# Optimization experiments

Hardware: AMD Instinct MI355X
Metric: run time of the kernel (lower is better)

## Reference

```python
import jax, jax.numpy as jnp
import numpy as np

NEG_INF = -9e15
NEG_SLOPE = 0.2

def setup_inputs() -> dict:
    key = jax.random.key(0)
    k1, k2, k3, k4 = jax.random.split(key, 4)
    N, d_in, d_out = 8192, 256, 256
    x = jax.random.normal(k1, (N, d_in), dtype=jnp.float32)
    adj = jax.random.randint(k2, (N, N), 0, 2).astype(jnp.float32)
    W = jax.random.normal(k3, (d_in, d_out), dtype=jnp.float32) * (1.0 / np.sqrt(d_in))
    a = jax.random.normal(k4, (2 * d_out,), dtype=jnp.float32) * (1.0 / np.sqrt(2 * d_out))
    return {"x": x, "adj": adj, "W": W, "a": a}

def reference(x, adj, W, a):
    d_out = W.shape[1]
    Wh = x @ W                                   # [N, d_out]
    # a([Wh_i || Wh_j]) decomposed: e_ij = <a_src, Wh_i> + <a_dst, Wh_j>
    e_src = Wh @ a[:d_out]                       # [N]
    e_dst = Wh @ a[d_out:]                       # [N]
    e = jax.nn.leaky_relu(e_src[:, None] + e_dst[None, :], NEG_SLOPE)  # [N, N]
    N = Wh.shape[0]
    mask = (adj > 0) | jnp.eye(N, dtype=bool)
    e = jnp.where(mask, e, NEG_INF)
    alpha = jax.nn.softmax(e, axis=1)            # [N, N]
    h = alpha @ Wh                               # [N, d_out]
    return h
```

## Files before the change

kernel.cpp:

```cpp
#include <hip/hip_runtime.h>
#include <stdint.h>

#define N 8192
#define D 256

typedef __attribute__((ext_vector_type(4))) float f32x4;
typedef __attribute__((ext_vector_type(8))) short bf16x8;

__device__ __forceinline__ unsigned short f2bf(float f) {
    unsigned u = __float_as_uint(f);
    u += 0x7fff + ((u >> 16) & 1);
    return (unsigned short)(u >> 16);
}
__device__ __forceinline__ float bf2f(unsigned short h) {
    unsigned u = ((unsigned)h) << 16;
    return __uint_as_float(u);
}
__device__ __forceinline__ float leaky(float x) {
    return fmaxf(x, 0.f) + 0.2f * fminf(x, 0.f);
}
__device__ __forceinline__ void sync_lds() {
    asm volatile("s_waitcnt lgkmcnt(0)\n\ts_barrier" ::: "memory");
}

__global__ __launch_bounds__(256) void k0_compress(const float* __restrict__ adj,
                                                   unsigned int* __restrict__ mask) {
    const size_t fbase = ((size_t)blockIdx.x * 256 + threadIdx.x) * 4;
    float4 v = *(const float4*)(adj + fbase);
    const int lane = threadIdx.x & 63;
    unsigned nib = (v.x > 0.f ? 1u : 0u) | (v.y > 0.f ? 2u : 0u) |
                   (v.z > 0.f ? 4u : 0u) | (v.w > 0.f ? 8u : 0u);
    unsigned word = nib << ((lane & 7) * 4);
    word |= __shfl_xor(word, 1);
    word |= __shfl_xor(word, 2);
    word |= __shfl_xor(word, 4);
    if ((lane & 7) == 0) {
        size_t widx = fbase >> 5;
        int r = (int)(widx >> 8);
        int ww = (int)(widx & 255);
        if ((r >> 5) == ww) word |= 1u << (r & 31);
        mask[widx] = word;
    }
}

__global__ __launch_bounds__(256) void k1c_x(const float* __restrict__ x,
                                             unsigned short* __restrict__ xhi,
                                             unsigned short* __restrict__ xlo) {
    const size_t idx = ((size_t)blockIdx.x * 256 + threadIdx.x) * 4;
    float4 v = *(const float4*)(x + idx);
    unsigned short h[4], l[4];
    float vv[4] = {v.x, v.y, v.z, v.w};
#pragma unroll
    for (int j = 0; j < 4; ++j) {
        h[j] = f2bf(vv[j]);
        l[j] = f2bf(vv[j] - bf2f(h[j]));
    }
    *(ushort4*)(xhi + idx) = *(ushort4*)h;
    *(ushort4*)(xlo + idx) = *(ushort4*)l;
}

__global__ __launch_bounds__(256) void k1w(const float* __restrict__ W,
                                           unsigned short* __restrict__ wthi,
                                           unsigned short* __restrict__ wtlo) {
    const int n = blockIdx.x;
    const int k = threadIdx.x;
    float w = W[(size_t)k * D + n];
    unsigned short h = f2bf(w);
    unsigned short l = f2bf(w - bf2f(h));
    wthi[(size_t)n * D + k] = h;
    wtlo[(size_t)n * D + k] = l;
}

__global__ __launch_bounds__(256) void k1m(const unsigned short* __restrict__ xhi,
                                           const unsigned short* __restrict__ xlo,
                                           const unsigned short* __restrict__ wthi,
                                           const unsigned short* __restrict__ wtlo,
                                           const float* __restrict__ a,
                                           unsigned short* __restrict__ WhT,
                                           float* __restrict__ e_src,
                                           float* __restrict__ e_dst) {
    __shared__ float obuf[16 * 256];

    const int t = threadIdx.x;
    const int r0 = blockIdx.x * 16;
    const int w = t >> 6;
    const int lane = t & 63;
    const int quad = lane >> 4, lo = lane & 15;

    const unsigned short* xh_row = xhi + (size_t)(r0 + lo) * D;
    const unsigned short* xl_row = xlo + (size_t)(r0 + lo) * D;

    f32x4 acc[4];
#pragma unroll
    for (int nt = 0; nt < 4; ++nt) acc[nt] = (f32x4){0.f, 0.f, 0.f, 0.f};

#pragma unroll
    for (int ks = 0; ks < 8; ++ks) {
        const int kofs = ks * 32 + quad * 8;
        bf16x8 ah = *(const bf16x8*)(xh_row + kofs);
        bf16x8 al = *(const bf16x8*)(xl_row + kofs);
#pragma unroll
        for (int nt = 0; nt < 4; ++nt) {
            const int n = w * 64 + nt * 16 + lo;
            bf16x8 bh = *(const bf16x8*)(wthi + (size_t)n * D + kofs);
            bf16x8 bl = *(const bf16x8*)(wtlo + (size_t)n * D + kofs);
            acc[nt] = __builtin_amdgcn_mfma_f32_16x16x32_bf16(ah, bh, acc[nt], 0, 0, 0);
            acc[nt] = __builtin_amdgcn_mfma_f32_16x16x32_bf16(ah, bl, acc[nt], 0, 0, 0);
            acc[nt] = __builtin_amdgcn_mfma_f32_16x16x32_bf16(al, bh, acc[nt], 0, 0, 0);
        }
    }

#pragma unroll
    for (int nt = 0; nt < 4; ++nt) {
        const int n = w * 64 + nt * 16 + lo;
        unsigned short pk[4];
#pragma unroll
        for (int reg = 0; reg < 4; ++reg) pk[reg] = f2bf(acc[nt][reg]);
        *(ushort2*)(WhT + (size_t)n * N + r0 + quad * 4) = *(ushort2*)&pk[0];
        *(ushort2*)(WhT + (size_t)n * N + r0 + quad * 4 + 2) = *(ushort2*)&pk[2];
    }

#pragma unroll
    for (int nt = 0; nt < 4; ++nt) {
        const int col = w * 64 + nt * 16 + lo;
#pragma unroll
        for (int reg = 0; reg < 4; ++reg)
            obuf[(quad * 4 + reg) * 256 + col] = acc[nt][reg];
    }
    __syncthreads();

    const int row = t >> 4;
    const int c0 = (t & 15) * 16;
    float ps = 0.f, pd = 0.f;
#pragma unroll
    for (int j = 0; j < 4; ++j) {
        float4 wv = *(const float4*)&obuf[row * 256 + c0 + j * 4];
        float4 as = *(const float4*)(a + c0 + j * 4);
        float4 ad = *(const float4*)(a + D + c0 + j * 4);
        ps += wv.x * as.x + wv.y * as.y + wv.z * as.z + wv.w * as.w;
        pd += wv.x * ad.x + wv.y * ad.y + wv.z * ad.z + wv.w * ad.w;
    }
#pragma unroll
    for (int msk = 1; msk < 16; msk <<= 1) {
        ps += __shfl_xor(ps, msk);
        pd += __shfl_xor(pd, msk);
    }
    if ((t & 15) == 0) {
        e_src[r0 + row] = ps;
        e_dst[r0 + row] = pd;
    }
}

__global__ __launch_bounds__(256) void k3_max(const float* __restrict__ e_dst,
                                              float* __restrict__ maxdst) {
    __shared__ float red[4];
    const int t = threadIdx.x;
    float m = -3.4e38f;
    for (int i = t; i < N; i += 256) m = fmaxf(m, e_dst[i]);
#pragma unroll
    for (int msk = 1; msk < 64; msk <<= 1) m = fmaxf(m, __shfl_xor(m, msk));
    if ((t & 63) == 0) red[t >> 6] = m;
    __syncthreads();
    if (t == 0) *maxdst = fmaxf(fmaxf(red[0], red[1]), fmaxf(red[2], red[3]));
}

#define BM 64
#define BK 64
#define RB (N / BM)
#define SPLITS 8
#define NITER ((N / SPLITS) / BK)
#define PSTRIDE 72
__global__ __launch_bounds__(512, 4) void k4_main(const unsigned char* __restrict__ mask,
                                                  const unsigned short* __restrict__ WhT,
                                                  const float* __restrict__ e_src,
                                                  const float* __restrict__ e_dst,
                                                  const float* __restrict__ maxdst,
                                                  float* __restrict__ O_part,
                                                  float* __restrict__ l_part) {
    __shared__ unsigned short p_lds[2][BM][PSTRIDE];

    const int t = threadIdx.x;
    const int rb = blockIdx.x & (RB - 1);
    const int s  = blockIdx.x >> 7;
    const int r0 = rb * BM;
    const int j0 = s * (N / SPLITS);

    const int pr = t >> 3;
    const int pcw = t & 7;
    const int pc = pcw * 8;
    const int gr = r0 + pr;

    const int w = t >> 6;
    const int lane = t & 63;
    const int quad = lane >> 4, lo = lane & 15;

    const float md = *maxdst;
    const float es = e_src[gr];
    const float m = leaky(es + md);

    f32x4 acc[4][2];
#pragma unroll
    for (int mt = 0; mt < 4; ++mt)
#pragma unroll
        for (int nt = 0; nt < 2; ++nt)
            acc[mt][nt] = (f32x4){0.f, 0.f, 0.f, 0.f};
    float lsum = 0.f;

    const unsigned char* mrow = mask + (size_t)gr * (N / 8) + (j0 >> 3) + pcw;
    const float* ed_row = e_dst + j0 + pc;
    const unsigned short* wt_base = WhT + (size_t)(w * 32 + lo) * N + j0 + quad * 8;

    unsigned int mb;
    float4 edv0, edv1;
    bf16x8 bfr[2][2];

    mb = mrow[0];
    edv0 = *(const float4*)(ed_row);
    edv1 = *(const float4*)(ed_row + 4);
#pragma unroll
    for (int ks2 = 0; ks2 < 2; ++ks2)
#pragma unroll
        for (int nt = 0; nt < 2; ++nt)
            bfr[ks2][nt] = *(const bf16x8*)(wt_base + (size_t)nt * (16 * N) + ks2 * 32);

    auto stage = [&](int buf) {
        float ev[8] = {edv0.x, edv0.y, edv0.z, edv0.w,
                       edv1.x, edv1.y, edv1.z, edv1.w};
        unsigned short pk[8];
#pragma unroll
        for (int jj = 0; jj < 8; ++jj) {
            float e = leaky(es + ev[jj]);
            float p = ((mb >> jj) & 1u) ? __expf(e - m) : 0.f;
            lsum += p;
            pk[jj] = f2bf(p);
        }
        *(uint4*)&p_lds[buf][pr][pc] = *(uint4*)pk;
    };

    stage(0);
    mb = mrow[8];
    edv0 = *(const float4*)(ed_row + BK);
    edv1 = *(const float4*)(ed_row + BK + 4);
    sync_lds();

#pragma unroll 2
    for (int it = 0; it < NITER; ++it) {
        const int cb = it & 1, nb = cb ^ 1;

#pragma unroll
        for (int ks2 = 0; ks2 < 2; ++ks2) {
            bf16x8 afr[4];
#pragma unroll
            for (int mt = 0; mt < 4; ++mt)
                afr[mt] = *(const bf16x8*)&p_lds[cb][mt * 16 + lo][ks2 * 32 + quad * 8];
#pragma unroll
            for (int nt = 0; nt < 2; ++nt)
#pragma unroll
                for (int mt = 0; mt < 4; ++mt)
                    acc[mt][nt] = __builtin_amdgcn_mfma_f32_16x16x32_bf16(
                        afr[mt], bfr[ks2][nt], acc[mt][nt], 0, 0, 0);
        }

        {
            const int itn = (it + 1 < NITER) ? it + 1 : NITER - 1;
#pragma unroll
            for (int ks2 = 0; ks2 < 2; ++ks2)
#pragma unroll
                for (int nt = 0; nt < 2; ++nt)
                    bfr[ks2][nt] = *(const bf16x8*)(wt_base + (size_t)nt * (16 * N) +
                                                    itn * BK + ks2 * 32);
        }

        if (it + 1 < NITER) {
            stage(nb);
            const int itn2 = (it + 2 < NITER) ? it + 2 : NITER - 1;
            mb = mrow[itn2 * 8];
            edv0 = *(const float4*)(ed_row + itn2 * BK);
            edv1 = *(const float4*)(ed_row + itn2 * BK + 4);
        }
        sync_lds();
    }

#pragma unroll
    for (int msk = 1; msk < 8; msk <<= 1) lsum += __shfl_xor(lsum, msk);
    if ((t & 7) == 0) l_part[(size_t)s * N + gr] = lsum;

    float* obuf = (float*)p_lds;
#pragma unroll
    for (int mt = 0; mt < 4; ++mt) {
        __syncthreads();
#pragma unroll
        for (int nt = 0; nt < 2; ++nt) {
            f32x4 v = acc[mt][nt];
            int col = w * 32 + nt * 16 + lo;
#pragma unroll
            for (int reg = 0; reg < 4; ++reg)
                obuf[(quad * 4 + reg) * 256 + col] = v[reg];
        }
        __syncthreads();
        const int orow = t >> 5;
        const int ocol = (t & 31) * 8;
        f32x4 o0 = *(const f32x4*)&obuf[orow * 256 + ocol];
        f32x4 o1 = *(const f32x4*)&obuf[orow * 256 + ocol + 4];
        float* dst = O_part + ((size_t)s * N + r0 + mt * 16 + orow) * D + ocol;
        *(f32x4*)dst = o0;
        *(f32x4*)(dst + 4) = o1;
    }
}

__global__ __launch_bounds__(256) void k5_reduce(const float* __restrict__ O_part,
                                                 const float* __restrict__ l_part,
                                                 float* __restrict__ out) {
    const int idx = blockIdx.x * 256 + threadIdx.x;
    const int r = idx >> 6;
    float lsum = 0.f;
#pragma unroll
    for (int s = 0; s < SPLITS; ++s) lsum += l_part[(size_t)s * N + r];
    f32x4 o = (f32x4){0.f, 0.f, 0.f, 0.f};
#pragma unroll
    for (int s = 0; s < SPLITS; ++s)
        o += *(const f32x4*)(O_part + (size_t)s * N * D + (size_t)idx * 4);
    const float inv = 1.f / lsum;
    *(f32x4*)(out + (size_t)idx * 4) = o * inv;
}

extern "C" void kernel_launch(void* const* d_in, const int* in_sizes, int n_in,
                              void* d_out, int out_size, void* d_ws, size_t ws_size,
                              hipStream_t stream) {
    const float* x   = (const float*)d_in[0];
    const float* adj = (const float*)d_in[1];
    const float* W   = (const float*)d_in[2];
    const float* a   = (const float*)d_in[3];
    float* out = (float*)d_out;

    char* ws = (char*)d_ws;
    unsigned short* xhi  = (unsigned short*)(ws);
    unsigned short* xlo  = (unsigned short*)(ws + 4194304);
    unsigned short* WhT  = (unsigned short*)(ws + 8388608);
    unsigned short* wthi = (unsigned short*)(ws + 12582912);
    unsigned short* wtlo = (unsigned short*)(ws + 12713984);
    float* e_src         = (float*)(ws + 12845056);
    float* e_dst         = (float*)(ws + 12877824);
    float* maxdst        = (float*)(ws + 12910592);
    float* l_part        = (float*)(ws + 12910848);
    unsigned int* mask   = (unsigned int*)(ws + 13631488);
    float* O_part        = (float*)(ws + 25165824);

    k0_compress<<<N * N / 4 / 256, 256, 0, stream>>>(adj, mask);
    k1c_x<<<N * D / 4 / 256, 256, 0, stream>>>(x, xhi, xlo);
    k1w<<<D, D, 0, stream>>>(W, wthi, wtlo);
    k1m<<<N / 16, 256, 0, stream>>>(xhi, xlo, wthi, wtlo, a, WhT, e_src, e_dst);
    k3_max<<<1, 256, 0, stream>>>(e_dst, maxdst);
    k4_main<<<RB * SPLITS, 512, 0, stream>>>((const unsigned char*)mask, WhT, e_src, e_dst,
                                             maxdst, O_part, l_part);
    k5_reduce<<<N * D / 4 / 256, 256, 0, stream>>>(O_part, l_part, out);
}
```

Baseline: 482.8 us.

## Merge prep kernels, fuse x split and max reduction, retile attention kernel

Folds the adjacency bitmask compression and the W transpose/split into one prep kernel. The x hi/lo bf16 split moves inside the projection GEMM, and the separate max-reduction kernel is replaced by a per-block atomicMax on an order-preserving float key. The main attention kernel drops from 64-row to 32-row tiles and from 8 to 4 column splits, which halves the partial-output traffic but doubles the number of row blocks and rereads of WhT. This cuts launch count and the intermediate x buffers, at the cost of a different occupancy and reuse balance in the main kernel.

```diff
diff --git a/kernel.cpp b/kernel.cpp
--- a/kernel.cpp
+++ b/kernel.cpp
@@ -13,73 +13,70 @@
     return (unsigned short)(u >> 16);
 }
 __device__ __forceinline__ float bf2f(unsigned short h) {
-    unsigned u = ((unsigned)h) << 16;
-    return __uint_as_float(u);
+    return __uint_as_float(((unsigned)h) << 16);
 }
 __device__ __forceinline__ float leaky(float x) {
     return fmaxf(x, 0.f) + 0.2f * fminf(x, 0.f);
 }
+__device__ __forceinline__ unsigned fkey(float f) {
+    unsigned b = __float_as_uint(f);
+    return (b & 0x80000000u) ? ~b : (b | 0x80000000u);
+}
+__device__ __forceinline__ float fkey_dec(unsigned k) {
+    unsigned b = (k & 0x80000000u) ? (k ^ 0x80000000u) : ~k;
+    return __uint_as_float(b);
+}
 __device__ __forceinline__ void sync_lds() {
     asm volatile("s_waitcnt lgkmcnt(0)\n\ts_barrier" ::: "memory");
 }
 
-__global__ __launch_bounds__(256) void k0_compress(const float* __restrict__ adj,
-                                                   unsigned int* __restrict__ mask) {
-    const size_t fbase = ((size_t)blockIdx.x * 256 + threadIdx.x) * 4;
-    float4 v = *(const float4*)(adj + fbase);
-    const int lane = threadIdx.x & 63;
-    unsigned nib = (v.x > 0.f ? 1u : 0u) | (v.y > 0.f ? 2u : 0u) |
-                   (v.z > 0.f ? 4u : 0u) | (v.w > 0.f ? 8u : 0u);
-    unsigned word = nib << ((lane & 7) * 4);
-    word |= __shfl_xor(word, 1);
-    word |= __shfl_xor(word, 2);
-    word |= __shfl_xor(word, 4);
-    if ((lane & 7) == 0) {
-        size_t widx = fbase >> 5;
-        int r = (int)(widx >> 8);
-        int ww = (int)(widx & 255);
-        if ((r >> 5) == ww) word |= 1u << (r & 31);
-        mask[widx] = word;
-    }
-}
-
-__global__ __launch_bounds__(256) void k1c_x(const float* __restrict__ x,
-                                             unsigned short* __restrict__ xhi,
-                                             unsigned short* __restrict__ xlo) {
-    const size_t idx = ((size_t)blockIdx.x * 256 + threadIdx.x) * 4;
-    float4 v = *(const float4*)(x + idx);
-    unsigned short h[4], l[4];
-    float vv[4] = {v.x, v.y, v.z, v.w};
-#pragma unroll
-    for (int j = 0; j < 4; ++j) {
-        h[j] = f2bf(vv[j]);
-        l[j] = f2bf(vv[j] - bf2f(h[j]));
-    }
-    *(ushort4*)(xhi + idx) = *(ushort4*)h;
-    *(ushort4*)(xlo + idx) = *(ushort4*)l;
-}
-
-__global__ __launch_bounds__(256) void k1w(const float* __restrict__ W,
-                                           unsigned short* __restrict__ wthi,
-                                           unsigned short* __restrict__ wtlo) {
-    const int n = blockIdx.x;
-    const int k = threadIdx.x;
-    float w = W[(size_t)k * D + n];
-    unsigned short h = f2bf(w);
-    unsigned short l = f2bf(w - bf2f(h));
-    wthi[(size_t)n * D + k] = h;
-    wtlo[(size_t)n * D + k] = l;
-}
-
-__global__ __launch_bounds__(256) void k1m(const unsigned short* __restrict__ xhi,
-                                           const unsigned short* __restrict__ xlo,
+#define NB_MASK (N * N / 4 / 256)
+__global__ __launch_bounds__(256) void kprep(const float* __restrict__ adj,
+                                             unsigned int* __restrict__ mask,
+                                             const float* __restrict__ W,
+                                             unsigned short* __restrict__ wthi,
+                                             unsigned short* __restrict__ wtlo,
+                                             unsigned int* __restrict__ maxkey) {
+    const int bid = blockIdx.x;
+    if (bid < NB_MASK) {
+        const size_t fbase = ((size_t)bid * 256 + threadIdx.x) * 4;
+        float4 v = *(const float4*)(adj + fbase);
+        const int lane = threadIdx.x & 63;
+        unsigned nib = (v.x > 0.f ? 1u : 0u) | (v.y > 0.f ? 2u : 0u) |
+                       (v.z > 0.f ? 4u : 0u) | (v.w > 0.f ? 8u : 0u);
+        unsigned word = nib << ((lane & 7) * 4);
+        word |= __shfl_xor(word, 1);
+        word |= __shfl_xor(word, 2);
+        word |= __shfl_xor(word, 4);
+        if ((lane & 7) == 0) {
+            size_t widx = fbase >> 5;
+            int r = (int)(widx >> 8);
+            int ww = (int)(widx & 255);
+            if ((r >> 5) == ww) word |= 1u << (r & 31);
+            mask[widx] = word;
+        }
+    } else {
+        const int n = bid - NB_MASK;
+        const int k = threadIdx.x;
+        if (n == 0 && k == 0) *maxkey = 0u;
+        float w = W[(size_t)k * D + n];
+        unsigned short h = f2bf(w);
+        unsigned short l = f2bf(w - bf2f(h));
+        wthi[(size_t)n * D + k] = h;
+        wtlo[(size_t)n * D + k] = l;
+    }
+}
+
+__global__ __launch_bounds__(256) void k1m(const float* __restrict__ x,
                                            const unsigned short* __restrict__ wthi,
                                            const unsigned short* __restrict__ wtlo,
                                            const float* __restrict__ a,
                                            unsigned short* __restrict__ WhT,
                                            float* __restrict__ e_src,
-                                           float* __restrict__ e_dst) {
+                                           float* __restrict__ e_dst,
+                                           unsigned int* __restrict__ maxkey) {
     __shared__ float obuf[16 * 256];
+    __shared__ float red[16];
 
     const int t = threadIdx.x;
     const int r0 = blockIdx.x * 16;
@@ -87,8 +84,7 @@
     const int lane = t & 63;
     const int quad = lane >> 4, lo = lane & 15;
 
-    const unsigned short* xh_row = xhi + (size_t)(r0 + lo) * D;
-    const unsigned short* xl_row = xlo + (size_t)(r0 + lo) * D;
+    const float* x_row = x + (size_t)(r0 + lo) * D;
 
     f32x4 acc[4];
 #pragma unroll
@@ -97,8 +93,16 @@
 #pragma unroll
     for (int ks = 0; ks < 8; ++ks) {
         const int kofs = ks * 32 + quad * 8;
-        bf16x8 ah = *(const bf16x8*)(xh_row + kofs);
-        bf16x8 al = *(const bf16x8*)(xl_row + kofs);
+        float4 v0 = *(const float4*)(x_row + kofs);
+        float4 v1 = *(const float4*)(x_row + kofs + 4);
+        float vv[8] = {v0.x, v0.y, v0.z, v0.w, v1.x, v1.y, v1.z, v1.w};
+        bf16x8 ah, al;
+#pragma unroll
+        for (int j = 0; j < 8; ++j) {
+            unsigned short h = f2bf(vv[j]);
+            ah[j] = (short)h;
+            al[j] = (short)f2bf(vv[j] - bf2f(h));
+        }
 #pragma unroll
         for (int nt = 0; nt < 4; ++nt) {
             const int n = w * 64 + nt * 16 + lo;
@@ -148,75 +152,72 @@
     if ((t & 15) == 0) {
         e_src[r0 + row] = ps;
         e_dst[r0 + row] = pd;
-    }
-}
-
-__global__ __launch_bounds__(256) void k3_max(const float* __restrict__ e_dst,
-                                              float* __restrict__ maxdst) {
-    __shared__ float red[4];
-    const int t = threadIdx.x;
-    float m = -3.4e38f;
-    for (int i = t; i < N; i += 256) m = fmaxf(m, e_dst[i]);
-#pragma unroll
-    for (int msk = 1; msk < 64; msk <<= 1) m = fmaxf(m, __shfl_xor(m, msk));
-    if ((t & 63) == 0) red[t >> 6] = m;
+        red[row] = pd;
+    }
     __syncthreads();
-    if (t == 0) *maxdst = fmaxf(fmaxf(red[0], red[1]), fmaxf(red[2], red[3]));
-}
-
-#define BM 64
+    if (t == 0) {
+        float m = red[0];
+#pragma unroll
+        for (int i = 1; i < 16; ++i) m = fmaxf(m, red[i]);
+        atomicMax(maxkey, fkey(m));
+    }
+}
+
+#define BM 32
 #define BK 64
 #define RB (N / BM)
-#define SPLITS 8
+#define SPLITS 4
 #define NITER ((N / SPLITS) / BK)
 #define PSTRIDE 72
 __global__ __launch_bounds__(512, 4) void k4_main(const unsigned char* __restrict__ mask,
                                                   const unsigned short* __restrict__ WhT,
                                                   const float* __restrict__ e_src,
                                                   const float* __restrict__ e_dst,
-                                                  const float* __restrict__ maxdst,
+                                                  const unsigned int* __restrict__ maxkey,
                                                   float* __restrict__ O_part,
                                                   float* __restrict__ l_part) {
-    __shared__ unsigned short p_lds[2][BM][PSTRIDE];
+    __shared__ char smem[16 * 256 * 4];
+    typedef unsigned short pbuf_t[BM][PSTRIDE];
+    pbuf_t* p_lds = (pbuf_t*)smem;
 
     const int t = threadIdx.x;
     const int rb = blockIdx.x & (RB - 1);
-    const int s  = blockIdx.x >> 7;
+    const int s  = blockIdx.x >> 8;
     const int r0 = rb * BM;
     const int j0 = s * (N / SPLITS);
 
-    const int pr = t >> 3;
-    const int pcw = t & 7;
-    const int pc = pcw * 8;
+    const int pr = t >> 4;
+    const int pcl = t & 15;
+    const int pc = pcl * 4;
     const int gr = r0 + pr;
 
     const int w = t >> 6;
     const int lane = t & 63;
     const int quad = lane >> 4, lo = lane & 15;
 
-    const float md = *maxdst;
+    const float md = fkey_dec(*maxkey);
     const float es = e_src[gr];
     const float m = leaky(es + md);
 
-    f32x4 acc[4][2];
-#pragma unroll
-    for (int mt = 0; mt < 4; ++mt)
+    f32x4 acc[2][2];
+#pragma unroll
+    for (int mt = 0; mt < 2; ++mt)
 #pragma unroll
         for (int nt = 0; nt < 2; ++nt)
             acc[mt][nt] = (f32x4){0.f, 0.f, 0.f, 0.f};
     float lsum = 0.f;
 
-    const unsigned char* mrow = mask + (size_t)gr * (N / 8) + (j0 >> 3) + pcw;
+    const unsigned char* mrow = mask + (size_t)gr * (N / 8) + (j0 >> 3) + (pcl >> 1);
+    const int nsh = (pcl & 1) * 4;
     const float* ed_row = e_dst + j0 + pc;
     const unsigned short* wt_base = WhT + (size_t)(w * 32 + lo) * N + j0 + quad * 8;
 
     unsigned int mb;
-    float4 edv0, edv1;
+    float4 edv;
     bf16x8 bfr[2][2];
 
     mb = mrow[0];
-    edv0 = *(const float4*)(ed_row);
-    edv1 = *(const float4*)(ed_row + 4);
+    edv = *(const float4*)(ed_row);
 #pragma unroll
     for (int ks2 = 0; ks2 < 2; ++ks2)
 #pragma unroll
@@ -224,23 +225,22 @@
             bfr[ks2][nt] = *(const bf16x8*)(wt_base + (size_t)nt * (16 * N) + ks2 * 32);
 
     auto stage = [&](int buf) {
-        float ev[8] = {edv0.x, edv0.y, edv0.z, edv0.w,
-                       edv1.x, edv1.y, edv1.z, edv1.w};
-        unsigned short pk[8];
-#pragma unroll
-        for (int jj = 0; jj < 8; ++jj) {
+        float ev[4] = {edv.x, edv.y, edv.z, edv.w};
+        unsigned nib = (mb >> nsh) & 0xFu;
+        unsigned short pk[4];
+#pragma unroll
+        for (int jj = 0; jj < 4; ++jj) {
             float e = leaky(es + ev[jj]);
-            float p = ((mb >> jj) & 1u) ? __expf(e - m) : 0.f;
+            float p = ((nib >> jj) & 1u) ? __expf(e - m) : 0.f;
             lsum += p;
             pk[jj] = f2bf(p);
         }
-        *(uint4*)&p_lds[buf][pr][pc] = *(uint4*)pk;
+        *(ushort4*)&p_lds[buf][pr][pc] = *(ushort4*)pk;
     };
 
     stage(0);
     mb = mrow[8];
-    edv0 = *(const float4*)(ed_row + BK);
-    edv1 = *(const float4*)(ed_row + BK + 4);
+    edv = *(const float4*)(ed_row + BK);
     sync_lds();
 
 #pragma unroll 2
@@ -249,14 +249,14 @@
 
 #pragma unroll
         for (int ks2 = 0; ks2 < 2; ++ks2) {
-            bf16x8 afr[4];
-#pragma unroll
-            for (int mt = 0; mt < 4; ++mt)
+            bf16x8 afr[2];
+#pragma unroll
+            for (int mt = 0; mt < 2; ++mt)
                 afr[mt] = *(const bf16x8*)&p_lds[cb][mt * 16 + lo][ks2 * 32 + quad * 8];
 #pragma unroll
             for (int nt = 0; nt < 2; ++nt)
 #pragma unroll
-                for (int mt = 0; mt < 4; ++mt)
+                for (int mt = 0; mt < 2; ++mt)
                     acc[mt][nt] = __builtin_amdgcn_mfma_f32_16x16x32_bf16(
                         afr[mt], bfr[ks2][nt], acc[mt][nt], 0, 0, 0);
         }
@@ -275,19 +275,18 @@
             stage(nb);
             const int itn2 = (it + 2 < NITER) ? it + 2 : NITER - 1;
             mb = mrow[itn2 * 8];
-            edv0 = *(const float4*)(ed_row + itn2 * BK);
-            edv1 = *(const float4*)(ed_row + itn2 * BK + 4);
+            edv = *(const float4*)(ed_row + itn2 * BK);
         }
         sync_lds();
     }
 
 #pragma unroll
-    for (int msk = 1; msk < 8; msk <<= 1) lsum += __shfl_xor(lsum, msk);
-    if ((t & 7) == 0) l_part[(size_t)s * N + gr] = lsum;
-
-    float* obuf = (float*)p_lds;
-#pragma unroll
-    for (int mt = 0; mt < 4; ++mt) {
+    for (int msk = 1; msk < 16; msk <<= 1) lsum += __shfl_xor(lsum, msk);
+    if ((t & 15) == 0) l_part[(size_t)s * N + gr] = lsum;
+
+    float* obuf = (float*)smem;
+#pragma unroll
+    for (int mt = 0; mt < 2; ++mt) {
         __syncthreads();
 #pragma unroll
         for (int nt = 0; nt < 2; ++nt) {
@@ -334,24 +333,19 @@
     float* out = (float*)d_out;
 
     char* ws = (char*)d_ws;
-    unsigned short* xhi  = (unsigned short*)(ws);
-    unsigned short* xlo  = (unsigned short*)(ws + 4194304);
-    unsigned short* WhT  = (unsigned short*)(ws + 8388608);
-    unsigned short* wthi = (unsigned short*)(ws + 12582912);
-    unsigned short* wtlo = (unsigned short*)(ws + 12713984);
-    float* e_src         = (float*)(ws + 12845056);
-    float* e_dst         = (float*)(ws + 12877824);
-    float* maxdst        = (float*)(ws + 12910592);
-    float* l_part        = (float*)(ws + 12910848);
-    unsigned int* mask   = (unsigned int*)(ws + 13631488);
-    float* O_part        = (float*)(ws + 25165824);
-
-    k0_compress<<<N * N / 4 / 256, 256, 0, stream>>>(adj, mask);
-    k1c_x<<<N * D / 4 / 256, 256, 0, stream>>>(x, xhi, xlo);
-    k1w<<<D, D, 0, stream>>>(W, wthi, wtlo);
-    k1m<<<N / 16, 256, 0, stream>>>(xhi, xlo, wthi, wtlo, a, WhT, e_src, e_dst);
-    k3_max<<<1, 256, 0, stream>>>(e_dst, maxdst);
+    unsigned short* WhT  = (unsigned short*)(ws);
+    unsigned short* wthi = (unsigned short*)(ws + 4194304);
+    unsigned short* wtlo = (unsigned short*)(ws + 4325376);
+    float* e_src         = (float*)(ws + 4456448);
+    float* e_dst         = (float*)(ws + 4489216);
+    unsigned int* maxkey = (unsigned int*)(ws + 4521984);
+    float* l_part        = (float*)(ws + 4522240);
+    unsigned int* mask   = (unsigned int*)(ws + 8388608);
+    float* O_part        = (float*)(ws + 16777216);
+
+    kprep<<<NB_MASK + D, 256, 0, stream>>>(adj, mask, W, wthi, wtlo, maxkey);
+    k1m<<<N / 16, 256, 0, stream>>>(x, wthi, wtlo, a, WhT, e_src, e_dst, maxkey);
     k4_main<<<RB * SPLITS, 512, 0, stream>>>((const unsigned char*)mask, WhT, e_src, e_dst,
-                                             maxdst, O_part, l_part);
+                                             maxkey, O_part, l_part);
     k5_reduce<<<N * D / 4 / 256, 256, 0, stream>>>(O_part, l_part, out);
 }
```

Result: slower. 517.5 us (+7.2%).
